# Optimization experiments

Measured on AMD Instinct MI355X. Metric: run time of the kernel, lower is better.

## Reference

```python
import jax, jax.numpy as jnp
import numpy as np

# --- static config / quantization scales (simulating the torch-int modules) ---
B, S, E, H = 2, 2048, 2048, 16
D = E // H  # head_dim = 128
CATTN_ALPHA = 0.004   # W8A8B8O8Conv1D requant scale: int32 acc -> int8 out
QK_ALPHA = 1e-4       # BMM_S8T_S8N_F32T: s_q * s_k dequant scale -> fp32 logits
PV_ALPHA = 0.002      # BMM_S8T_S8N_S8T: (1/127)*s_v/s_out requant scale -> int8 out
PROJ_ALPHA = 0.003    # W8A8BFP32OFP32Conv1D dequant scale -> fp32 out


def q8(x):
    """round + saturate to int8 range (values kept in float32)."""
    return jnp.clip(jnp.round(x), -128.0, 127.0)


def setup_inputs() -> dict:
    key = jax.random.key(0)
    k0, k1, k2, k3, k4 = jax.random.split(key, 5)
    i8 = lambda k, shape: jax.random.randint(k, shape, -128, 128).astype(jnp.float32)
    return {
        "hidden_states": i8(k0, (B, S, E)),      # int8 activations (simulated)
        "w_attn": i8(k1, (E, 3 * E)),            # int8 c_attn weight (Conv1D: x @ W)
        "b_attn": i8(k2, (3 * E,)),              # int8 c_attn bias
        "w_proj": i8(k3, (E, E)),                # int8 c_proj weight
        "b_proj": jax.random.normal(k4, (E,), dtype=jnp.float32),  # fp32 c_proj bias
    }


def reference(hidden_states, w_attn, b_attn, w_proj, b_proj):
    # c_attn: W8A8B8O8 — int32 accumulate, requantize, add int8 bias, saturate
    qkv = q8(CATTN_ALPHA * jnp.matmul(hidden_states, w_attn) + b_attn)  # [B,S,3E] int8
    q, k, v = jnp.split(qkv, 3, axis=-1)

    def split_heads(t):  # [B,S,E] -> [B,H,S,D]
        return t.reshape(B, S, H, D).transpose(0, 2, 1, 3)

    q, k, v = split_heads(q), split_heads(k), split_heads(v)

    # qk_bmm: BMM_S8T_S8N_F32T -> fp32 logits, then /sqrt(head_dim)
    logits = QK_ALPHA * jnp.einsum("bhqd,bhkd->bhqk", q, k)
    logits = logits / jnp.float32(np.sqrt(D))

    # causal mask (tril bias buffer); masked positions -> dtype min
    causal = jnp.tril(jnp.ones((S, S), dtype=bool))
    mask_value = jnp.finfo(logits.dtype).min
    logits = jnp.where(causal[None, None], logits, mask_value)

    # softmax, then requantize probabilities to int8: round(p * 127)
    p = jax.nn.softmax(logits, axis=-1)
    p_i8 = q8(p * 127.0)  # [B,H,S,S] int8 (simulated)

    # pv_bmm: BMM_S8T_S8N_S8T -> int8 attn output
    attn_out = q8(PV_ALPHA * jnp.einsum("bhqk,bhkd->bhqd", p_i8, v))  # [B,H,S,D]

    # merge heads -> [B,S,E]
    attn_out = attn_out.transpose(0, 2, 1, 3).reshape(B, S, E)

    # c_proj: W8A8BFP32OFP32 — int32 accumulate, dequant to fp32, add fp32 bias
    out = PROJ_ALPHA * jnp.matmul(attn_out, w_proj) + b_proj  # [B,S,E] fp32
    return out
```

## Files before the change

kernel.cpp:

```cpp
#include <hip/hip_runtime.h>
#include <cstdint>
#include <cstddef>


typedef int v4i __attribute__((ext_vector_type(4)));

static constexpr float CATTN_ALPHA = 0.004f;
static constexpr float PV_ALPHA    = 0.002f;
static constexpr float PROJ_ALPHA  = 0.003f;
static constexpr float CE2   = 1.275174308e-05f;
static constexpr float MAGIC = 12582912.0f;

#define GLL16(gp, lp)                                              \
  __builtin_amdgcn_global_load_lds(                                \
      (const __attribute__((address_space(1))) void*)(gp),         \
      (__attribute__((address_space(3))) void*)(lp), 16, 0, 0)

__device__ __forceinline__ float exp2_fast(float x) {
#if __has_builtin(__builtin_amdgcn_exp2f)
  return __builtin_amdgcn_exp2f(x);
#else
  return __builtin_exp2f(x);
#endif
}

__device__ __forceinline__ uint32_t pack4(uint32_t u0, uint32_t u1, uint32_t u2,
                                          uint32_t u3) {
#if __has_builtin(__builtin_amdgcn_perm)
  uint32_t t01 = __builtin_amdgcn_perm(u1, u0, 0x00000400u);
  uint32_t t23 = __builtin_amdgcn_perm(u3, u2, 0x00000400u);
  return __builtin_amdgcn_perm(t23, t01, 0x05040100u);
#else
  return (u0 & 255u) | ((u1 & 255u) << 8) | ((u2 & 255u) << 16) | (u3 << 24);
#endif
}

__global__ __launch_bounds__(256) void quant_kernel(const float* __restrict__ src,
                                                    int8_t* __restrict__ dst, int n4) {
  int i = blockIdx.x * 256 + threadIdx.x;
  if (i >= n4) return;
  float4 v = reinterpret_cast<const float4*>(src)[i];
  int b0 = __float2int_rn(v.x) & 255;
  int b1 = __float2int_rn(v.y) & 255;
  int b2 = __float2int_rn(v.z) & 255;
  int b3 = __float2int_rn(v.w) & 255;
  reinterpret_cast<int*>(dst)[i] = b0 | (b1 << 8) | (b2 << 16) | (b3 << 24);
}

__global__ __launch_bounds__(256) void quant_transpose_kernel(const float* __restrict__ src,
                                                              int8_t* __restrict__ dst,
                                                              int K, int N) {
  __shared__ int8_t ts[64][68];
  const int k0 = blockIdx.x * 64, n0 = blockIdx.y * 64;
  const int t = threadIdx.x;
  for (int c = t; c < 1024; c += 256) {
    int r = c >> 4, cc = (c & 15) << 2;
    float4 v = *reinterpret_cast<const float4*>(&src[(size_t)(k0 + r) * N + n0 + cc]);
    int b0 = __float2int_rn(v.x) & 255;
    int b1 = __float2int_rn(v.y) & 255;
    int b2 = __float2int_rn(v.z) & 255;
    int b3 = __float2int_rn(v.w) & 255;
    *reinterpret_cast<int*>(&ts[r][cc]) = b0 | (b1 << 8) | (b2 << 16) | (b3 << 24);
  }
  __syncthreads();
  {
    int c = t;
    int rn = c >> 2, ck = (c & 3) << 4;
    __attribute__((aligned(16))) int8_t tmp[16];
#pragma unroll
    for (int j = 0; j < 16; ++j) tmp[j] = ts[ck + j][rn];
    *reinterpret_cast<v4i*>(&dst[(size_t)(n0 + rn) * K + k0 + ck]) =
        *reinterpret_cast<const v4i*>(tmp);
  }
}

__global__ __launch_bounds__(256) void gemm_cattn_kernel(
    const int8_t* __restrict__ A, const int8_t* __restrict__ BT,
    const float* __restrict__ bias,
    int8_t* __restrict__ qout, int8_t* __restrict__ kout, int8_t* __restrict__ vtout) {
  __shared__ __align__(16) int8_t As[2][128][64];
  __shared__ __align__(16) int8_t Bs[2][128][64];
  const int t = threadIdx.x;
  const int lane = t & 63, wave = t >> 6;
  const int wr = wave >> 1, wc = wave & 1;
  const int l15 = lane & 15, l4 = lane >> 4;
  const int m0 = blockIdx.y * 128, n0 = blockIdx.x * 128;

  const int srow = lane >> 2, scol = (lane & 3) << 4;
  const int8_t* ag = A + (size_t)(m0 + wave * 32 + srow) * 2048 + scol;
  const int8_t* bg = BT + (size_t)(n0 + wave * 32 + srow) * 2048 + scol;

  auto stage = [&](int b, int ki) {
    const int8_t* a_ = ag + ki * 64;
    GLL16(a_, &As[b][wave * 32][0]);
    GLL16(a_ + (size_t)16 * 2048, &As[b][wave * 32 + 16][0]);
    const int8_t* b_ = bg + ki * 64;
    GLL16(b_, &Bs[b][wave * 32][0]);
    GLL16(b_ + (size_t)16 * 2048, &Bs[b][wave * 32 + 16][0]);
  };

  v4i acc[4][4];
#pragma unroll
  for (int i = 0; i < 4; ++i)
#pragma unroll
    for (int j = 0; j < 4; ++j) acc[i][j] = (v4i){0, 0, 0, 0};

  stage(0, 0);
  __syncthreads();
  for (int ki = 0; ki < 32; ++ki) {
    if (ki < 31) stage((ki + 1) & 1, ki + 1);
    const int8_t* ab = &As[ki & 1][0][0];
    const int8_t* bb = &Bs[ki & 1][0][0];
    v4i af[4], bf[4];
#pragma unroll
    for (int i = 0; i < 4; ++i)
      af[i] = *reinterpret_cast<const v4i*>(ab + (wr * 64 + i * 16 + l15) * 64 + l4 * 16);
#pragma unroll
    for (int j = 0; j < 4; ++j)
      bf[j] = *reinterpret_cast<const v4i*>(bb + (wc * 64 + j * 16 + l15) * 64 + l4 * 16);
#pragma unroll
    for (int i = 0; i < 4; ++i)
#pragma unroll
      for (int j = 0; j < 4; ++j)
        acc[i][j] = __builtin_amdgcn_mfma_i32_16x16x64_i8(af[i], bf[j], acc[i][j], 0, 0, 0);
    __syncthreads();
  }

  const int which = n0 >> 11;
  const int hh = (n0 & 2047) >> 7;
  const int bi = m0 >> 11;
  const int s_base = m0 & 2047;
  float bv[4];
#pragma unroll
  for (int j = 0; j < 4; ++j) bv[j] = bias[n0 + wc * 64 + j * 16 + l15];

  if (which == 2) {
    int8_t* vb = vtout + ((size_t)(bi * 16 + hh) * 128) * 2048;
#pragma unroll
    for (int i = 0; i < 4; ++i) {
#pragma unroll
      for (int j = 0; j < 4; ++j) {
        uint32_t w = 0;
#pragma unroll
        for (int rr = 0; rr < 4; ++rr) {
          float f = __fadd_rn(__fmul_rn(CATTN_ALPHA, (float)acc[i][j][rr]), bv[j]);
          f = rintf(f);
          f = fminf(fmaxf(f, -128.f), 127.f);
          w |= ((uint32_t)((int)f & 255)) << (rr * 8);
        }
        int d = wc * 64 + j * 16 + l15;
        int s0i = s_base + wr * 64 + i * 16 + l4 * 4;
        *reinterpret_cast<uint32_t*>(vb + (size_t)d * 2048 + s0i) = w;
      }
    }
  } else {
    int8_t* dst = (which == 0) ? qout : kout;
    int8_t* db = dst + ((size_t)(bi * 16 + hh) * 2048 + s_base) * 128;
#pragma unroll
    for (int i = 0; i < 4; ++i)
#pragma unroll
      for (int j = 0; j < 4; ++j)
#pragma unroll
        for (int rr = 0; rr < 4; ++rr) {
          float f = __fadd_rn(__fmul_rn(CATTN_ALPHA, (float)acc[i][j][rr]), bv[j]);
          f = rintf(f);
          f = fminf(fmaxf(f, -128.f), 127.f);
          int mo = wr * 64 + i * 16 + l4 * 4 + rr;
          int d = wc * 64 + j * 16 + l15;
          db[(size_t)mo * 128 + d] = (int8_t)(int)f;
        }
  }
}

__global__ __launch_bounds__(256) void gemm_cproj_kernel(
    const int8_t* __restrict__ A, const int8_t* __restrict__ BT,
    const float* __restrict__ bias, float* __restrict__ out) {
  __shared__ __align__(16) int8_t As[2][128][64];
  __shared__ __align__(16) int8_t Bs[2][128][64];
  const int t = threadIdx.x;
  const int lane = t & 63, wave = t >> 6;
  const int wr = wave >> 1, wc = wave & 1;
  const int l15 = lane & 15, l4 = lane >> 4;
  const int m0 = blockIdx.y * 128, n0 = blockIdx.x * 128;

  const int srow = lane >> 2, scol = (lane & 3) << 4;
  const int8_t* ag = A + (size_t)(m0 + wave * 32 + srow) * 2048 + scol;
  const int8_t* bg = BT + (size_t)(n0 + wave * 32 + srow) * 2048 + scol;

  auto stage = [&](int b, int ki) {
    const int8_t* a_ = ag + ki * 64;
    GLL16(a_, &As[b][wave * 32][0]);
    GLL16(a_ + (size_t)16 * 2048, &As[b][wave * 32 + 16][0]);
    const int8_t* b_ = bg + ki * 64;
    GLL16(b_, &Bs[b][wave * 32][0]);
    GLL16(b_ + (size_t)16 * 2048, &Bs[b][wave * 32 + 16][0]);
  };

  v4i acc[4][4];
#pragma unroll
  for (int i = 0; i < 4; ++i)
#pragma unroll
    for (int j = 0; j < 4; ++j) acc[i][j] = (v4i){0, 0, 0, 0};

  stage(0, 0);
  __syncthreads();
  for (int ki = 0; ki < 32; ++ki) {
    if (ki < 31) stage((ki + 1) & 1, ki + 1);
    const int8_t* ab = &As[ki & 1][0][0];
    const int8_t* bb = &Bs[ki & 1][0][0];
    v4i af[4], bf[4];
#pragma unroll
    for (int i = 0; i < 4; ++i)
      af[i] = *reinterpret_cast<const v4i*>(ab + (wr * 64 + i * 16 + l15) * 64 + l4 * 16);
#pragma unroll
    for (int j = 0; j < 4; ++j)
      bf[j] = *reinterpret_cast<const v4i*>(bb + (wc * 64 + j * 16 + l15) * 64 + l4 * 16);
#pragma unroll
    for (int i = 0; i < 4; ++i)
#pragma unroll
      for (int j = 0; j < 4; ++j)
        acc[i][j] = __builtin_amdgcn_mfma_i32_16x16x64_i8(af[i], bf[j], acc[i][j], 0, 0, 0);
    __syncthreads();
  }
#pragma unroll
  for (int i = 0; i < 4; ++i)
#pragma unroll
    for (int j = 0; j < 4; ++j)
#pragma unroll
      for (int rr = 0; rr < 4; ++rr) {
        int m = m0 + wr * 64 + i * 16 + l4 * 4 + rr;
        int n = n0 + wc * 64 + j * 16 + l15;
        out[(size_t)m * 2048 + n] =
            __fadd_rn(__fmul_rn(PROJ_ALPHA, (float)acc[i][j][rr]), bias[n]);
      }
}

__global__ __launch_bounds__(256) void attn_kernel(
    const int8_t* __restrict__ Q, const int8_t* __restrict__ K8,
    const int8_t* __restrict__ VT, int8_t* __restrict__ O) {
  __shared__ __align__(16) int8_t q_s[64][128];
  __shared__ __align__(16) int8_t k_s[2][64][128];
  __shared__ __align__(16) int8_t vt_s[2][128][64];
  __shared__ __align__(16) int8_t p_s[64][80];

  const int t = threadIdx.x;
  const int lane = t & 63, wave = t >> 6;
  const int l15 = lane & 15, l4 = lane >> 4;
  const int bh = blockIdx.x;
  const int qt = (int)gridDim.y - 1 - (int)blockIdx.y;
  const int r0 = qt * 64;
  const size_t kqbase = (size_t)bh * (2048 * 128);
  const size_t vtbase = (size_t)bh * (128 * 2048);

  const int kq_go = ((lane >> 3) << 7) + ((((lane & 7) ^ (lane >> 3)) & 7) << 4);
  const int vt_go = ((lane >> 2) * 2048) + ((lane & 3) << 4);
  const int koff0 = (l15 << 7) + ((((0 + l4) ^ l15) & 7) << 4);
  const int koff1 = (l15 << 7) + ((((4 + l4) ^ l15) & 7) << 4);
  const int voff = l15 * 64 + l4 * 16;
  const int poff_w = (wave * 16 + l15) * 80 + l4 * 4;
  const int poff_r = (wave * 16 + l15) * 80 + l4 * 16;

  {
    const int8_t* qg = Q + kqbase + (size_t)(r0 + wave * 16) * 128 + kq_go;
    GLL16(qg, &q_s[wave * 16][0]);
    GLL16(qg + 8 * 128, &q_s[wave * 16 + 8][0]);
    const int8_t* kg = K8 + kqbase + (size_t)(wave * 16) * 128 + kq_go;
    GLL16(kg, &k_s[0][wave * 16][0]);
    GLL16(kg + 8 * 128, &k_s[0][wave * 16 + 8][0]);
  }
  __syncthreads();

  const v4i qf0 = *reinterpret_cast<const v4i*>(&q_s[0][0] + wave * 2048 + koff0);
  const v4i qf1 = *reinterpret_cast<const v4i*>(&q_s[0][0] + wave * 2048 + koff1);
  const int qgl = wave * 16 + l15;

  float acc_l[4] = {0.f, 0.f, 0.f, 0.f};

  for (int tt = 0; tt <= qt; ++tt) {
    if (tt < qt) {
      const int8_t* kg =
          K8 + kqbase + (size_t)((tt + 1) * 64 + wave * 16) * 128 + kq_go;
      GLL16(kg, &k_s[(tt + 1) & 1][wave * 16][0]);
      GLL16(kg + 8 * 128, &k_s[(tt + 1) & 1][wave * 16 + 8][0]);
    }
    const int8_t* kb = &k_s[tt & 1][0][0];
    v4i sacc[4];
#pragma unroll
    for (int ni = 0; ni < 4; ++ni) sacc[ni] = (v4i){0, 0, 0, 0};
#pragma unroll
    for (int ni = 0; ni < 4; ++ni) {
      v4i ak = *reinterpret_cast<const v4i*>(kb + ni * 2048 + koff0);
      sacc[ni] = __builtin_amdgcn_mfma_i32_16x16x64_i8(ak, qf0, sacc[ni], 0, 0, 0);
    }
#pragma unroll
    for (int ni = 0; ni < 4; ++ni) {
      v4i ak = *reinterpret_cast<const v4i*>(kb + ni * 2048 + koff1);
      sacc[ni] = __builtin_amdgcn_mfma_i32_16x16x64_i8(ak, qf1, sacc[ni], 0, 0, 0);
    }
    if (tt < qt) {
#pragma unroll
      for (int ni = 0; ni < 4; ++ni)
#pragma unroll
        for (int rr = 0; rr < 4; ++rr)
          acc_l[rr] += exp2_fast(CE2 * (float)sacc[ni][rr]);
    } else {
#pragma unroll
      for (int ni = 0; ni < 4; ++ni)
#pragma unroll
        for (int rr = 0; rr < 4; ++rr) {
          float e = exp2_fast(CE2 * (float)sacc[ni][rr]);
          acc_l[rr] += (ni * 16 + l4 * 4 + rr <= qgl) ? e : 0.f;
        }
    }
    __syncthreads();
  }
  float l_run = (acc_l[0] + acc_l[1]) + (acc_l[2] + acc_l[3]);
  l_run += __shfl_xor(l_run, 16);
  l_run += __shfl_xor(l_run, 32);
  const float inv = 127.0f / l_run;

  {
    const int8_t* kg = K8 + kqbase + (size_t)(wave * 16) * 128 + kq_go;
    GLL16(kg, &k_s[0][wave * 16][0]);
    GLL16(kg + 8 * 128, &k_s[0][wave * 16 + 8][0]);
    const int8_t* vg = VT + vtbase + (size_t)(wave * 32) * 2048 + vt_go;
    GLL16(vg, &vt_s[0][wave * 32][0]);
    GLL16(vg + (size_t)16 * 2048, &vt_s[0][wave * 32 + 16][0]);
  }
  __syncthreads();

  v4i oacc[8];
#pragma unroll
  for (int nj = 0; nj < 8; ++nj) oacc[nj] = (v4i){0, 0, 0, 0};

  for (int tt = 0; tt <= qt; ++tt) {
    if (tt < qt) {
      const int kb1 = (tt + 1) * 64;
      const int8_t* kg = K8 + kqbase + (size_t)(kb1 + wave * 16) * 128 + kq_go;
      GLL16(kg, &k_s[(tt + 1) & 1][wave * 16][0]);
      GLL16(kg + 8 * 128, &k_s[(tt + 1) & 1][wave * 16 + 8][0]);
      const int8_t* vg = VT + vtbase + (size_t)(wave * 32) * 2048 + kb1 + vt_go;
      GLL16(vg, &vt_s[(tt + 1) & 1][wave * 32][0]);
      GLL16(vg + (size_t)16 * 2048, &vt_s[(tt + 1) & 1][wave * 32 + 16][0]);
    }
    const int8_t* kb = &k_s[tt & 1][0][0];
    v4i sacc[4];
#pragma unroll
    for (int ni = 0; ni < 4; ++ni) sacc[ni] = (v4i){0, 0, 0, 0};
#pragma unroll
    for (int ni = 0; ni < 4; ++ni) {
      v4i ak = *reinterpret_cast<const v4i*>(kb + ni * 2048 + koff0);
      sacc[ni] = __builtin_amdgcn_mfma_i32_16x16x64_i8(ak, qf0, sacc[ni], 0, 0, 0);
    }
#pragma unroll
    for (int ni = 0; ni < 4; ++ni) {
      v4i ak = *reinterpret_cast<const v4i*>(kb + ni * 2048 + koff1);
      sacc[ni] = __builtin_amdgcn_mfma_i32_16x16x64_i8(ak, qf1, sacc[ni], 0, 0, 0);
    }
    if (tt < qt) {
#pragma unroll
      for (int ni = 0; ni < 4; ++ni) {
        float f0 = fmaf(exp2_fast(CE2 * (float)sacc[ni][0]), inv, MAGIC);
        float f1 = fmaf(exp2_fast(CE2 * (float)sacc[ni][1]), inv, MAGIC);
        float f2 = fmaf(exp2_fast(CE2 * (float)sacc[ni][2]), inv, MAGIC);
        float f3 = fmaf(exp2_fast(CE2 * (float)sacc[ni][3]), inv, MAGIC);
        uint32_t w = pack4(__float_as_uint(f0), __float_as_uint(f1),
                           __float_as_uint(f2), __float_as_uint(f3));
        *reinterpret_cast<uint32_t*>(&p_s[0][0] + poff_w + ni * 16) = w;
      }
    } else {
#pragma unroll
      for (int ni = 0; ni < 4; ++ni) {
        float e0 = exp2_fast(CE2 * (float)sacc[ni][0]);
        float e1 = exp2_fast(CE2 * (float)sacc[ni][1]);
        float e2 = exp2_fast(CE2 * (float)sacc[ni][2]);
        float e3 = exp2_fast(CE2 * (float)sacc[ni][3]);
        int c = ni * 16 + l4 * 4;
        e0 = (c + 0 <= qgl) ? e0 : 0.f;
        e1 = (c + 1 <= qgl) ? e1 : 0.f;
        e2 = (c + 2 <= qgl) ? e2 : 0.f;
        e3 = (c + 3 <= qgl) ? e3 : 0.f;
        float f0 = fmaf(e0, inv, MAGIC), f1 = fmaf(e1, inv, MAGIC);
        float f2 = fmaf(e2, inv, MAGIC), f3 = fmaf(e3, inv, MAGIC);
        uint32_t w = pack4(__float_as_uint(f0), __float_as_uint(f1),
                           __float_as_uint(f2), __float_as_uint(f3));
        *reinterpret_cast<uint32_t*>(&p_s[0][0] + poff_w + ni * 16) = w;
      }
    }
    asm volatile("s_waitcnt lgkmcnt(0)" ::: "memory");
    v4i pf = *reinterpret_cast<const v4i*>(&p_s[0][0] + poff_r);
    const int8_t* vb = &vt_s[tt & 1][0][0];
#pragma unroll
    for (int nj = 0; nj < 8; ++nj) {
      v4i vf = *reinterpret_cast<const v4i*>(vb + nj * 1024 + voff);
      oacc[nj] = __builtin_amdgcn_mfma_i32_16x16x64_i8(pf, vf, oacc[nj], 0, 0, 0);
    }
    __syncthreads();
  }

  const int bq = bh >> 4, hh = bh & 15;
#pragma unroll
  for (int nj = 0; nj < 8; ++nj) {
#pragma unroll
    for (int rr = 0; rr < 4; ++rr) {
      int r = r0 + wave * 16 + l4 * 4 + rr;
      int d = nj * 16 + l15;
      float f = rintf(__fmul_rn(PV_ALPHA, (float)oacc[nj][rr]));
      f = fminf(fmaxf(f, -128.f), 127.f);
      O[((size_t)bq * 2048 + r) * 2048 + hh * 128 + d] = (int8_t)(int)f;
    }
  }
}

extern "C" void kernel_launch(void* const* d_in, const int* in_sizes, int n_in,
                              void* d_out, int out_size, void* d_ws, size_t ws_size,
                              hipStream_t stream) {
  const float* hs_f    = (const float*)d_in[0];
  const float* wattn_f = (const float*)d_in[1];
  const float* battn_f = (const float*)d_in[2];
  const float* wproj_f = (const float*)d_in[3];
  const float* bproj_f = (const float*)d_in[4];
  float* out_f = (float*)d_out;

  int8_t* ws = (int8_t*)d_ws;
  int8_t* hs_i8   = ws;
  int8_t* wT_attn = ws + 8388608;
  int8_t* wT_proj = ws + 20971520;
  int8_t* q_i8    = ws + 25165824;
  int8_t* k_i8    = ws + 33554432;
  int8_t* vT_i8   = ws + 41943040;
  int8_t* attn_i8 = ws + 50331648;

  quant_kernel<<<dim3(8192), dim3(256), 0, stream>>>(hs_f, hs_i8, 2097152);
  quant_transpose_kernel<<<dim3(32, 96), dim3(256), 0, stream>>>(wattn_f, wT_attn, 2048, 6144);
  quant_transpose_kernel<<<dim3(32, 32), dim3(256), 0, stream>>>(wproj_f, wT_proj, 2048, 2048);
  gemm_cattn_kernel<<<dim3(48, 32), dim3(256), 0, stream>>>(hs_i8, wT_attn, battn_f,
                                                            q_i8, k_i8, vT_i8);
  attn_kernel<<<dim3(32, 32), dim3(256), 0, stream>>>(q_i8, k_i8, vT_i8, attn_i8);
  gemm_cproj_kernel<<<dim3(16, 32), dim3(256), 0, stream>>>(attn_i8, wT_proj, bproj_f, out_f);
}
```

Before: 188.2 us.

## Double GEMM K-tile to 128 and XOR-swizzle LDS layout in both GEMMs

```diff
diff --git a/kernel.cpp b/kernel.cpp
--- a/kernel.cpp
+++ b/kernel.cpp
@@ -78,25 +78,27 @@
     const int8_t* __restrict__ A, const int8_t* __restrict__ BT,
     const float* __restrict__ bias,
     int8_t* __restrict__ qout, int8_t* __restrict__ kout, int8_t* __restrict__ vtout) {
-  __shared__ __align__(16) int8_t As[2][128][64];
-  __shared__ __align__(16) int8_t Bs[2][128][64];
+  __shared__ __align__(16) int8_t As[2][128][128];
+  __shared__ __align__(16) int8_t Bs[2][128][128];
   const int t = threadIdx.x;
   const int lane = t & 63, wave = t >> 6;
   const int wr = wave >> 1, wc = wave & 1;
   const int l15 = lane & 15, l4 = lane >> 4;
   const int m0 = blockIdx.y * 128, n0 = blockIdx.x * 128;
 
-  const int srow = lane >> 2, scol = (lane & 3) << 4;
+  const int srow = lane >> 3;
+  const int scol = ((lane & 7) ^ srow) << 4;
   const int8_t* ag = A + (size_t)(m0 + wave * 32 + srow) * 2048 + scol;
   const int8_t* bg = BT + (size_t)(n0 + wave * 32 + srow) * 2048 + scol;
 
   auto stage = [&](int b, int ki) {
-    const int8_t* a_ = ag + ki * 64;
-    GLL16(a_, &As[b][wave * 32][0]);
-    GLL16(a_ + (size_t)16 * 2048, &As[b][wave * 32 + 16][0]);
-    const int8_t* b_ = bg + ki * 64;
-    GLL16(b_, &Bs[b][wave * 32][0]);
-    GLL16(b_ + (size_t)16 * 2048, &Bs[b][wave * 32 + 16][0]);
+    const int8_t* a_ = ag + ki * 128;
+    const int8_t* b_ = bg + ki * 128;
+#pragma unroll
+    for (int g = 0; g < 4; ++g) {
+      GLL16(a_ + (size_t)(g * 8) * 2048, &As[b][wave * 32 + g * 8][0]);
+      GLL16(b_ + (size_t)(g * 8) * 2048, &Bs[b][wave * 32 + g * 8][0]);
+    }
   };
 
   v4i acc[4][4];
@@ -104,25 +106,32 @@
   for (int i = 0; i < 4; ++i)
 #pragma unroll
     for (int j = 0; j < 4; ++j) acc[i][j] = (v4i){0, 0, 0, 0};
+
+  const int rswz = (l4 ^ (l15 & 7)) << 4;
+  const int aoff = (wr * 64 + l15) * 128 + rswz;
+  const int boff = (wc * 64 + l15) * 128 + rswz;
 
   stage(0, 0);
   __syncthreads();
-  for (int ki = 0; ki < 32; ++ki) {
-    if (ki < 31) stage((ki + 1) & 1, ki + 1);
+  for (int ki = 0; ki < 16; ++ki) {
+    if (ki < 15) stage((ki + 1) & 1, ki + 1);
     const int8_t* ab = &As[ki & 1][0][0];
     const int8_t* bb = &Bs[ki & 1][0][0];
-    v4i af[4], bf[4];
-#pragma unroll
-    for (int i = 0; i < 4; ++i)
-      af[i] = *reinterpret_cast<const v4i*>(ab + (wr * 64 + i * 16 + l15) * 64 + l4 * 16);
-#pragma unroll
-    for (int j = 0; j < 4; ++j)
-      bf[j] = *reinterpret_cast<const v4i*>(bb + (wc * 64 + j * 16 + l15) * 64 + l4 * 16);
-#pragma unroll
-    for (int i = 0; i < 4; ++i)
+#pragma unroll
+    for (int ks = 0; ks < 2; ++ks) {
+      v4i af[4], bf[4];
+#pragma unroll
+      for (int i = 0; i < 4; ++i)
+        af[i] = *reinterpret_cast<const v4i*>(ab + ((aoff + i * 2048) ^ (ks * 64)));
 #pragma unroll
       for (int j = 0; j < 4; ++j)
-        acc[i][j] = __builtin_amdgcn_mfma_i32_16x16x64_i8(af[i], bf[j], acc[i][j], 0, 0, 0);
+        bf[j] = *reinterpret_cast<const v4i*>(bb + ((boff + j * 2048) ^ (ks * 64)));
+#pragma unroll
+      for (int i = 0; i < 4; ++i)
+#pragma unroll
+        for (int j = 0; j < 4; ++j)
+          acc[i][j] = __builtin_amdgcn_mfma_i32_16x16x64_i8(af[i], bf[j], acc[i][j], 0, 0, 0);
+    }
     __syncthreads();
   }
 
@@ -175,25 +184,27 @@
 __global__ __launch_bounds__(256) void gemm_cproj_kernel(
     const int8_t* __restrict__ A, const int8_t* __restrict__ BT,
     const float* __restrict__ bias, float* __restrict__ out) {
-  __shared__ __align__(16) int8_t As[2][128][64];
-  __shared__ __align__(16) int8_t Bs[2][128][64];
+  __shared__ __align__(16) int8_t As[2][128][128];
+  __shared__ __align__(16) int8_t Bs[2][128][128];
   const int t = threadIdx.x;
   const int lane = t & 63, wave = t >> 6;
   const int wr = wave >> 1, wc = wave & 1;
   const int l15 = lane & 15, l4 = lane >> 4;
   const int m0 = blockIdx.y * 128, n0 = blockIdx.x * 128;
 
-  const int srow = lane >> 2, scol = (lane & 3) << 4;
+  const int srow = lane >> 3;
+  const int scol = ((lane & 7) ^ srow) << 4;
   const int8_t* ag = A + (size_t)(m0 + wave * 32 + srow) * 2048 + scol;
   const int8_t* bg = BT + (size_t)(n0 + wave * 32 + srow) * 2048 + scol;
 
   auto stage = [&](int b, int ki) {
-    const int8_t* a_ = ag + ki * 64;
-    GLL16(a_, &As[b][wave * 32][0]);
-    GLL16(a_ + (size_t)16 * 2048, &As[b][wave * 32 + 16][0]);
-    const int8_t* b_ = bg + ki * 64;
-    GLL16(b_, &Bs[b][wave * 32][0]);
-    GLL16(b_ + (size_t)16 * 2048, &Bs[b][wave * 32 + 16][0]);
+    const int8_t* a_ = ag + ki * 128;
+    const int8_t* b_ = bg + ki * 128;
+#pragma unroll
+    for (int g = 0; g < 4; ++g) {
+      GLL16(a_ + (size_t)(g * 8) * 2048, &As[b][wave * 32 + g * 8][0]);
+      GLL16(b_ + (size_t)(g * 8) * 2048, &Bs[b][wave * 32 + g * 8][0]);
+    }
   };
 
   v4i acc[4][4];
@@ -201,25 +212,32 @@
   for (int i = 0; i < 4; ++i)
 #pragma unroll
     for (int j = 0; j < 4; ++j) acc[i][j] = (v4i){0, 0, 0, 0};
+
+  const int rswz = (l4 ^ (l15 & 7)) << 4;
+  const int aoff = (wr * 64 + l15) * 128 + rswz;
+  const int boff = (wc * 64 + l15) * 128 + rswz;
 
   stage(0, 0);
   __syncthreads();
-  for (int ki = 0; ki < 32; ++ki) {
-    if (ki < 31) stage((ki + 1) & 1, ki + 1);
+  for (int ki = 0; ki < 16; ++ki) {
+    if (ki < 15) stage((ki + 1) & 1, ki + 1);
     const int8_t* ab = &As[ki & 1][0][0];
     const int8_t* bb = &Bs[ki & 1][0][0];
-    v4i af[4], bf[4];
-#pragma unroll
-    for (int i = 0; i < 4; ++i)
-      af[i] = *reinterpret_cast<const v4i*>(ab + (wr * 64 + i * 16 + l15) * 64 + l4 * 16);
-#pragma unroll
-    for (int j = 0; j < 4; ++j)
-      bf[j] = *reinterpret_cast<const v4i*>(bb + (wc * 64 + j * 16 + l15) * 64 + l4 * 16);
-#pragma unroll
-    for (int i = 0; i < 4; ++i)
+#pragma unroll
+    for (int ks = 0; ks < 2; ++ks) {
+      v4i af[4], bf[4];
+#pragma unroll
+      for (int i = 0; i < 4; ++i)
+        af[i] = *reinterpret_cast<const v4i*>(ab + ((aoff + i * 2048) ^ (ks * 64)));
 #pragma unroll
       for (int j = 0; j < 4; ++j)
-        acc[i][j] = __builtin_amdgcn_mfma_i32_16x16x64_i8(af[i], bf[j], acc[i][j], 0, 0, 0);
+        bf[j] = *reinterpret_cast<const v4i*>(bb + ((boff + j * 2048) ^ (ks * 64)));
+#pragma unroll
+      for (int i = 0; i < 4; ++i)
+#pragma unroll
+        for (int j = 0; j < 4; ++j)
+          acc[i][j] = __builtin_amdgcn_mfma_i32_16x16x64_i8(af[i], bf[j], acc[i][j], 0, 0, 0);
+    }
     __syncthreads();
   }
 #pragma unroll
```

After: 170.0 us. 1.11x faster.

## Load GEMM fragments directly from global and vectorize epilogue stores via swapped MFMA operands

Applied to the files above, without the earlier changes.

```diff
diff --git a/kernel.cpp b/kernel.cpp
--- a/kernel.cpp
+++ b/kernel.cpp
@@ -33,6 +33,13 @@
 #else
   return (u0 & 255u) | ((u1 & 255u) << 8) | ((u2 & 255u) << 16) | (u3 << 24);
 #endif
+}
+
+__device__ __forceinline__ uint32_t rq8(float alpha, int a, float b) {
+  float f = __fadd_rn(__fmul_rn(alpha, (float)a), b);
+  f = rintf(f);
+  f = fminf(fmaxf(f, -128.f), 127.f);
+  return (uint32_t)((int)f) & 255u;
 }
 
 __global__ __launch_bounds__(256) void quant_kernel(const float* __restrict__ src,
@@ -78,26 +85,14 @@
     const int8_t* __restrict__ A, const int8_t* __restrict__ BT,
     const float* __restrict__ bias,
     int8_t* __restrict__ qout, int8_t* __restrict__ kout, int8_t* __restrict__ vtout) {
-  __shared__ __align__(16) int8_t As[2][128][64];
-  __shared__ __align__(16) int8_t Bs[2][128][64];
   const int t = threadIdx.x;
   const int lane = t & 63, wave = t >> 6;
   const int wr = wave >> 1, wc = wave & 1;
   const int l15 = lane & 15, l4 = lane >> 4;
   const int m0 = blockIdx.y * 128, n0 = blockIdx.x * 128;
 
-  const int srow = lane >> 2, scol = (lane & 3) << 4;
-  const int8_t* ag = A + (size_t)(m0 + wave * 32 + srow) * 2048 + scol;
-  const int8_t* bg = BT + (size_t)(n0 + wave * 32 + srow) * 2048 + scol;
-
-  auto stage = [&](int b, int ki) {
-    const int8_t* a_ = ag + ki * 64;
-    GLL16(a_, &As[b][wave * 32][0]);
-    GLL16(a_ + (size_t)16 * 2048, &As[b][wave * 32 + 16][0]);
-    const int8_t* b_ = bg + ki * 64;
-    GLL16(b_, &Bs[b][wave * 32][0]);
-    GLL16(b_ + (size_t)16 * 2048, &Bs[b][wave * 32 + 16][0]);
-  };
+  const int8_t* ap = A + (size_t)(m0 + wr * 64 + l15) * 2048 + l4 * 16;
+  const int8_t* bp = BT + (size_t)(n0 + wc * 64 + l15) * 2048 + l4 * 16;
 
   v4i acc[4][4];
 #pragma unroll
@@ -105,25 +100,25 @@
 #pragma unroll
     for (int j = 0; j < 4; ++j) acc[i][j] = (v4i){0, 0, 0, 0};
 
-  stage(0, 0);
-  __syncthreads();
-  for (int ki = 0; ki < 32; ++ki) {
-    if (ki < 31) stage((ki + 1) & 1, ki + 1);
-    const int8_t* ab = &As[ki & 1][0][0];
-    const int8_t* bb = &Bs[ki & 1][0][0];
-    v4i af[4], bf[4];
+  for (int kt = 0; kt < 2048; kt += 128) {
+    v4i af[4][2], bf[4][2];
 #pragma unroll
     for (int i = 0; i < 4; ++i)
-      af[i] = *reinterpret_cast<const v4i*>(ab + (wr * 64 + i * 16 + l15) * 64 + l4 * 16);
+#pragma unroll
+      for (int ks = 0; ks < 2; ++ks)
+        af[i][ks] = *reinterpret_cast<const v4i*>(ap + kt + (size_t)i * (16 * 2048) + ks * 64);
 #pragma unroll
     for (int j = 0; j < 4; ++j)
-      bf[j] = *reinterpret_cast<const v4i*>(bb + (wc * 64 + j * 16 + l15) * 64 + l4 * 16);
-#pragma unroll
-    for (int i = 0; i < 4; ++i)
-#pragma unroll
-      for (int j = 0; j < 4; ++j)
-        acc[i][j] = __builtin_amdgcn_mfma_i32_16x16x64_i8(af[i], bf[j], acc[i][j], 0, 0, 0);
-    __syncthreads();
+#pragma unroll
+      for (int ks = 0; ks < 2; ++ks)
+        bf[j][ks] = *reinterpret_cast<const v4i*>(bp + kt + (size_t)j * (16 * 2048) + ks * 64);
+#pragma unroll
+    for (int ks = 0; ks < 2; ++ks)
+#pragma unroll
+      for (int i = 0; i < 4; ++i)
+#pragma unroll
+        for (int j = 0; j < 4; ++j)
+          acc[i][j] = __builtin_amdgcn_mfma_i32_16x16x64_i8(af[i][ks], bf[j][ks], acc[i][j], 0, 0, 0);
   }
 
   const int which = n0 >> 11;
@@ -140,14 +135,10 @@
     for (int i = 0; i < 4; ++i) {
 #pragma unroll
       for (int j = 0; j < 4; ++j) {
-        uint32_t w = 0;
-#pragma unroll
-        for (int rr = 0; rr < 4; ++rr) {
-          float f = __fadd_rn(__fmul_rn(CATTN_ALPHA, (float)acc[i][j][rr]), bv[j]);
-          f = rintf(f);
-          f = fminf(fmaxf(f, -128.f), 127.f);
-          w |= ((uint32_t)((int)f & 255)) << (rr * 8);
-        }
+        uint32_t w = pack4(rq8(CATTN_ALPHA, acc[i][j][0], bv[j]),
+                           rq8(CATTN_ALPHA, acc[i][j][1], bv[j]),
+                           rq8(CATTN_ALPHA, acc[i][j][2], bv[j]),
+                           rq8(CATTN_ALPHA, acc[i][j][3], bv[j]));
         int d = wc * 64 + j * 16 + l15;
         int s0i = s_base + wr * 64 + i * 16 + l4 * 4;
         *reinterpret_cast<uint32_t*>(vb + (size_t)d * 2048 + s0i) = w;
@@ -175,26 +166,14 @@
 __global__ __launch_bounds__(256) void gemm_cproj_kernel(
     const int8_t* __restrict__ A, const int8_t* __restrict__ BT,
     const float* __restrict__ bias, float* __restrict__ out) {
-  __shared__ __align__(16) int8_t As[2][128][64];
-  __shared__ __align__(16) int8_t Bs[2][128][64];
   const int t = threadIdx.x;
   const int lane = t & 63, wave = t >> 6;
   const int wr = wave >> 1, wc = wave & 1;
   const int l15 = lane & 15, l4 = lane >> 4;
   const int m0 = blockIdx.y * 128, n0 = blockIdx.x * 128;
 
-  const int srow = lane >> 2, scol = (lane & 3) << 4;
-  const int8_t* ag = A + (size_t)(m0 + wave * 32 + srow) * 2048 + scol;
-  const int8_t* bg = BT + (size_t)(n0 + wave * 32 + srow) * 2048 + scol;
-
-  auto stage = [&](int b, int ki) {
-    const int8_t* a_ = ag + ki * 64;
-    GLL16(a_, &As[b][wave * 32][0]);
-    GLL16(a_ + (size_t)16 * 2048, &As[b][wave * 32 + 16][0]);
-    const int8_t* b_ = bg + ki * 64;
-    GLL16(b_, &Bs[b][wave * 32][0]);
-    GLL16(b_ + (size_t)16 * 2048, &Bs[b][wave * 32 + 16][0]);
-  };
+  const int8_t* ap = A + (size_t)(m0 + wr * 64 + l15) * 2048 + l4 * 16;
+  const int8_t* bp = BT + (size_t)(n0 + wc * 64 + l15) * 2048 + l4 * 16;
 
   v4i acc[4][4];
 #pragma unroll
@@ -202,37 +181,41 @@
 #pragma unroll
     for (int j = 0; j < 4; ++j) acc[i][j] = (v4i){0, 0, 0, 0};
 
-  stage(0, 0);
-  __syncthreads();
-  for (int ki = 0; ki < 32; ++ki) {
-    if (ki < 31) stage((ki + 1) & 1, ki + 1);
-    const int8_t* ab = &As[ki & 1][0][0];
-    const int8_t* bb = &Bs[ki & 1][0][0];
-    v4i af[4], bf[4];
+  for (int kt = 0; kt < 2048; kt += 128) {
+    v4i af[4][2], bf[4][2];
 #pragma unroll
     for (int i = 0; i < 4; ++i)
-      af[i] = *reinterpret_cast<const v4i*>(ab + (wr * 64 + i * 16 + l15) * 64 + l4 * 16);
+#pragma unroll
+      for (int ks = 0; ks < 2; ++ks)
+        af[i][ks] = *reinterpret_cast<const v4i*>(ap + kt + (size_t)i * (16 * 2048) + ks * 64);
 #pragma unroll
     for (int j = 0; j < 4; ++j)
-      bf[j] = *reinterpret_cast<const v4i*>(bb + (wc * 64 + j * 16 + l15) * 64 + l4 * 16);
-#pragma unroll
-    for (int i = 0; i < 4; ++i)
-#pragma unroll
-      for (int j = 0; j < 4; ++j)
-        acc[i][j] = __builtin_amdgcn_mfma_i32_16x16x64_i8(af[i], bf[j], acc[i][j], 0, 0, 0);
-    __syncthreads();
-  }
-#pragma unroll
-  for (int i = 0; i < 4; ++i)
-#pragma unroll
-    for (int j = 0; j < 4; ++j)
-#pragma unroll
-      for (int rr = 0; rr < 4; ++rr) {
-        int m = m0 + wr * 64 + i * 16 + l4 * 4 + rr;
-        int n = n0 + wc * 64 + j * 16 + l15;
-        out[(size_t)m * 2048 + n] =
-            __fadd_rn(__fmul_rn(PROJ_ALPHA, (float)acc[i][j][rr]), bias[n]);
-      }
+#pragma unroll
+      for (int ks = 0; ks < 2; ++ks)
+        bf[j][ks] = *reinterpret_cast<const v4i*>(bp + kt + (size_t)j * (16 * 2048) + ks * 64);
+#pragma unroll
+    for (int ks = 0; ks < 2; ++ks)
+#pragma unroll
+      for (int i = 0; i < 4; ++i)
+#pragma unroll
+        for (int j = 0; j < 4; ++j)
+          acc[i][j] = __builtin_amdgcn_mfma_i32_16x16x64_i8(bf[j][ks], af[i][ks], acc[i][j], 0, 0, 0);
+  }
+#pragma unroll
+  for (int j = 0; j < 4; ++j) {
+    float4 b4 = *reinterpret_cast<const float4*>(&bias[n0 + wc * 64 + j * 16 + l4 * 4]);
+#pragma unroll
+    for (int i = 0; i < 4; ++i) {
+      int m = m0 + wr * 64 + i * 16 + l15;
+      int n = n0 + wc * 64 + j * 16 + l4 * 4;
+      float4 o;
+      o.x = __fadd_rn(__fmul_rn(PROJ_ALPHA, (float)acc[i][j][0]), b4.x);
+      o.y = __fadd_rn(__fmul_rn(PROJ_ALPHA, (float)acc[i][j][1]), b4.y);
+      o.z = __fadd_rn(__fmul_rn(PROJ_ALPHA, (float)acc[i][j][2]), b4.z);
+      o.w = __fadd_rn(__fmul_rn(PROJ_ALPHA, (float)acc[i][j][3]), b4.w);
+      *reinterpret_cast<float4*>(&out[(size_t)m * 2048 + n]) = o;
+    }
+  }
 }
 
 __global__ __launch_bounds__(256) void attn_kernel(
@@ -393,21 +376,22 @@
 #pragma unroll
     for (int nj = 0; nj < 8; ++nj) {
       v4i vf = *reinterpret_cast<const v4i*>(vb + nj * 1024 + voff);
-      oacc[nj] = __builtin_amdgcn_mfma_i32_16x16x64_i8(pf, vf, oacc[nj], 0, 0, 0);
+      oacc[nj] = __builtin_amdgcn_mfma_i32_16x16x64_i8(vf, pf, oacc[nj], 0, 0, 0);
     }
     __syncthreads();
   }
 
   const int bq = bh >> 4, hh = bh & 15;
-#pragma unroll
-  for (int nj = 0; nj < 8; ++nj) {
-#pragma unroll
-    for (int rr = 0; rr < 4; ++rr) {
-      int r = r0 + wave * 16 + l4 * 4 + rr;
-      int d = nj * 16 + l15;
-      float f = rintf(__fmul_rn(PV_ALPHA, (float)oacc[nj][rr]));
-      f = fminf(fmaxf(f, -128.f), 127.f);
-      O[((size_t)bq * 2048 + r) * 2048 + hh * 128 + d] = (int8_t)(int)f;
+  {
+    int r = r0 + wave * 16 + l15;
+    int8_t* ob = O + ((size_t)bq * 2048 + r) * 2048 + hh * 128;
+#pragma unroll
+    for (int nj = 0; nj < 8; ++nj) {
+      uint32_t w = pack4(rq8(PV_ALPHA, oacc[nj][0], 0.f),
+                         rq8(PV_ALPHA, oacc[nj][1], 0.f),
+                         rq8(PV_ALPHA, oacc[nj][2], 0.f),
+                         rq8(PV_ALPHA, oacc[nj][3], 0.f));
+      *reinterpret_cast<uint32_t*>(ob + nj * 16 + l4 * 4) = w;
     }
   }
 }
```

Result: slower. 323.2 us (+71.7%).
